# Kernel optimization log

Hardware: AMD Instinct MI355X
Metric: run time of the kernel (lower is better)

The kernel has to match this reference:

```python
import jax, jax.numpy as jnp
import numpy as np

ALPHA = 32.0 ** 2
MASK_VALUE = -jnp.finfo(jnp.float32).max


def rotate_half(t):
    d = t.shape[-1] // 2
    x1, x2 = t[..., :d], t[..., d:]
    return jnp.concatenate([-x2, x1], axis=-1)


def apply_rotary_pos_emb(freqs, t):
    # freqs: [n, rot_dim], t: [b, h, n, d]
    rot_dim = freqs.shape[-1]
    t_rot, t_pass = t[..., :rot_dim], t[..., rot_dim:]
    t_rot = t_rot * jnp.cos(freqs) + rotate_half(t_rot) * jnp.sin(freqs)
    return jnp.concatenate([t_rot, t_pass], axis=-1)


def stable_softmax(t, alpha=ALPHA):
    t = t / alpha
    t = t - jax.lax.stop_gradient(jnp.max(t, axis=-1, keepdims=True))
    return jax.nn.softmax(t * alpha, axis=-1)


def setup_inputs() -> dict:
    key = jax.random.key(0)
    ks = jax.random.split(key, 8)
    b, n, dim = 2, 2048, 1024
    h, dh = 16, 64
    inner = h * dh
    rot_dim = 32
    return {
        "x": jax.random.normal(ks[0], (b, n, dim), jnp.float32),
        "mask": jnp.ones((b, n), dtype=bool),
        "rotary_pos_emb": jax.random.normal(ks[1], (n, rot_dim), jnp.float32),
        "null_k": jax.random.normal(ks[2], (h, 1, dh), jnp.float32),
        "null_v": jax.random.normal(ks[3], (h, 1, dh), jnp.float32),
        "th_w": jax.random.normal(ks[4], (h, h), jnp.float32) * (1.0 / h),
        "w_q": jax.random.normal(ks[5], (dim, inner), jnp.float32) * (dim ** -0.5),
        "w_kv": jax.random.normal(ks[6], (dim, 2 * inner), jnp.float32) * (dim ** -0.5),
        "w_out": jax.random.normal(ks[7], (inner, dim), jnp.float32) * (inner ** -0.5),
        "b_out": jnp.zeros((dim,), jnp.float32),
    }


def reference(x, mask, rotary_pos_emb, null_k, null_v, th_w, w_q, w_kv, w_out, b_out):
    b, n, _ = x.shape
    h, _, dh = null_k.shape
    scale = dh ** -0.5

    q = x @ w_q                      # [b, n, h*dh]
    kv = x @ w_kv                    # [b, n, 2*h*dh]
    k, v = jnp.split(kv, 2, axis=-1)

    def to_heads(t):
        return t.reshape(b, n, h, dh).transpose(0, 2, 1, 3)  # [b, h, n, d]

    q, k, v = map(to_heads, (q, k, v))

    # rotary applied to q, k AND v (as in source)
    q = apply_rotary_pos_emb(rotary_pos_emb, q)
    k = apply_rotary_pos_emb(rotary_pos_emb, k)
    v = apply_rotary_pos_emb(rotary_pos_emb, v)

    # prepend learned null key/value token
    nk = jnp.broadcast_to(null_k[None], (b, h, 1, dh))
    nv = jnp.broadcast_to(null_v[None], (b, h, 1, dh))
    k = jnp.concatenate([nk, k], axis=2)  # [b, h, n+1, d]
    v = jnp.concatenate([nv, v], axis=2)

    q = q * scale
    sim = jnp.einsum('bhid,bhjd->bhij', q, k)  # [b, h, n, n+1]

    # key padding mask (null token always visible)
    key_mask = jnp.pad(mask, ((0, 0), (1, 0)), constant_values=True)
    sim = jnp.where(key_mask[:, None, None, :], sim, MASK_VALUE)

    # causal mask: padded col > row + (j - i)
    i, j = sim.shape[-2], sim.shape[-1]
    causal = jnp.arange(j)[None, :] > jnp.arange(i)[:, None] + (j - i)
    sim = jnp.where(causal, MASK_VALUE, sim)

    attn = stable_softmax(sim)
    # talking heads: 1x1 conv over head channel == head mixing matrix
    attn = jnp.einsum('gh,bhij->bgij', th_w, attn)

    out = jnp.einsum('bhij,bhjd->bhid', attn, v)
    out = out.transpose(0, 2, 1, 3).reshape(b, n, h * dh)
    return out @ w_out + b_out
```

## Files before the change

### kernel.cpp

```cpp
#include <hip/hip_runtime.h>
#include <hip/hip_bf16.h>
#include <cstdint>
#include <cstddef>

using bf16 = __hip_bfloat16;
typedef __attribute__((ext_vector_type(8))) short short8;
typedef __attribute__((ext_vector_type(4))) short short4v;
typedef __attribute__((ext_vector_type(4))) float f32x4;

constexpr int BB  = 2;
constexpr int SEQ = 2048;
constexpr int NH  = 16;
constexpr int HD  = 64;
constexpr int KPAD = 2112;
constexpr int DM  = 1024;

static __device__ __forceinline__ bf16 f2b(float v) { return __float2bfloat16(v); }
static __device__ __forceinline__ float b2f(bf16 v) { return __bfloat162float(v); }

static __device__ __forceinline__ void gload16(const bf16* g, bf16* l) {
  __builtin_amdgcn_global_load_lds(
      (const __attribute__((address_space(1))) void*)g,
      (__attribute__((address_space(3))) void*)l, 16, 0, 0);
}

__global__ __launch_bounds__(256) void cast_x_kernel(const float* __restrict__ src,
                                                     bf16* __restrict__ dst, int n4) {
  int idx = blockIdx.x * 256 + threadIdx.x;
  if (idx >= n4) return;
  float4 v = *(const float4*)(src + (size_t)idx * 4);
  bf16 o[4] = {f2b(v.x), f2b(v.y), f2b(v.z), f2b(v.w)};
  *(short4v*)(dst + (size_t)idx * 4) = *(short4v*)o;
}

__global__ __launch_bounds__(256) void zero_kernel(float* __restrict__ dst, int n4) {
  int idx = blockIdx.x * 256 + threadIdx.x;
  if (idx >= n4) return;
  float4 z; z.x = 0.f; z.y = 0.f; z.z = 0.f; z.w = 0.f;
  *(float4*)(dst + (size_t)idx * 4) = z;
}

__global__ __launch_bounds__(256) void cast_o_kernel(const float* __restrict__ src,
                                                     bf16* __restrict__ dst, int n4) {
  int idx = blockIdx.x * 256 + threadIdx.x;
  if (idx >= n4) return;
  float4 v = *(const float4*)(src + (size_t)idx * 4);
  bf16 o[4] = {f2b(v.x), f2b(v.y), f2b(v.z), f2b(v.w)};
  *(short4v*)(dst + (size_t)idx * 4) = *(short4v*)o;
}

__global__ __launch_bounds__(256) void transpose_cast_kernel(const float* __restrict__ src,
                                                             bf16* __restrict__ dst,
                                                             int colsN, int ldDst) {
  int n0 = blockIdx.x * 32, k0 = blockIdx.y * 32;
  __shared__ alignas(16) float t[32][33];
  int tid = threadIdx.x;
  {
    int r = tid >> 3, c4 = (tid & 7) * 4;
    float4 v = *(const float4*)(src + (size_t)(k0 + r) * colsN + n0 + c4);
    t[r][c4 + 0] = v.x; t[r][c4 + 1] = v.y; t[r][c4 + 2] = v.z; t[r][c4 + 3] = v.w;
  }
  __syncthreads();
  {
    int nl = tid >> 3, k4 = (tid & 7) * 4;
    bf16 o[4];
#pragma unroll
    for (int u = 0; u < 4; ++u) o[u] = f2b(t[k4 + u][nl]);
    *(short4v*)(dst + (size_t)(n0 + nl) * ldDst + k0 + k4) = *(short4v*)o;
  }
}

template <bool OUT_BF16, bool BIAS>
__global__ __launch_bounds__(256) void gemm_lds_kernel(
    const bf16* __restrict__ A, int lda,
    const bf16* __restrict__ BT, int ldb,
    void* __restrict__ Cv, int ldc,
    const float* __restrict__ bias, int K) {
  constexpr int BK = 32;
  const int tid = threadIdx.x, wave = tid >> 6, lane = tid & 63;
  const int lr = lane & 15, lq = lane >> 4;
  const int wm = wave >> 1, wn = wave & 1;
  const int m0 = blockIdx.y * 128, n0 = blockIdx.x * 128;
  const int srow = lane >> 2;
  const int scol = (lane & 3) * 8;

  __shared__ alignas(16) bf16 ash[128 * BK];
  __shared__ alignas(16) bf16 bsh[128 * BK];

  f32x4 acc[4][4];
#pragma unroll
  for (int i = 0; i < 4; ++i)
#pragma unroll
    for (int j = 0; j < 4; ++j)
#pragma unroll
      for (int r = 0; r < 4; ++r) acc[i][j][r] = 0.f;

  const int nk = K / BK;
  for (int kt = 0; kt < nk; ++kt) {
    const int k0 = kt * BK;
#pragma unroll
    for (int c = 0; c < 2; ++c) {
      const int rbase = wave * 32 + c * 16;
      gload16(A + (size_t)(m0 + rbase + srow) * lda + k0 + scol, ash + rbase * BK);
      gload16(BT + (size_t)(n0 + rbase + srow) * ldb + k0 + scol, bsh + rbase * BK);
    }
    __syncthreads();
    short8 af[4], bfv[4];
#pragma unroll
    for (int i = 0; i < 4; ++i)
      af[i] = *(const short8*)&ash[(wm * 64 + i * 16 + lr) * BK + lq * 8];
#pragma unroll
    for (int j = 0; j < 4; ++j)
      bfv[j] = *(const short8*)&bsh[(wn * 64 + j * 16 + lr) * BK + lq * 8];
#pragma unroll
    for (int i = 0; i < 4; ++i)
#pragma unroll
      for (int j = 0; j < 4; ++j)
        acc[i][j] = __builtin_amdgcn_mfma_f32_16x16x32_bf16(af[i], bfv[j], acc[i][j], 0, 0, 0);
    __syncthreads();
  }
#pragma unroll
  for (int i = 0; i < 4; ++i) {
    int row0 = m0 + wm * 64 + i * 16 + lq * 4;
#pragma unroll
    for (int j = 0; j < 4; ++j) {
      int col = n0 + wn * 64 + j * 16 + lr;
      float bv = BIAS ? bias[col] : 0.f;
#pragma unroll
      for (int r = 0; r < 4; ++r) {
        float v = acc[i][j][r] + bv;
        if (OUT_BF16) ((bf16*)Cv)[(size_t)(row0 + r) * ldc + col] = f2b(v);
        else          ((float*)Cv)[(size_t)(row0 + r) * ldc + col] = v;
      }
    }
  }
}

template <int BM, int BN, int BK, int WM, int WN, bool OUT_BF16, bool BIAS>
__global__ __launch_bounds__(WM * WN * 64) void gemm_bt_kernel(
    const bf16* __restrict__ A, int lda,
    const bf16* __restrict__ BT, int ldb,
    void* __restrict__ Cv, int ldc,
    const float* __restrict__ bias, int K) {
  constexpr int THREADS = WM * WN * 64;
  constexpr int FM = BM / (WM * 16), FN = BN / (WN * 16);
  const int tid = threadIdx.x;
  const int wave = tid >> 6, lane = tid & 63;
  const int lr = lane & 15, lq = lane >> 4;
  const int wm = wave / WN, wn = wave % WN;
  const int m0 = blockIdx.y * BM, n0 = blockIdx.x * BN;

  __shared__ alignas(16) bf16 ash[BM][BK + 8];
  __shared__ alignas(16) bf16 bsh[BN][BK + 8];

  f32x4 acc[FM][FN];
#pragma unroll
  for (int i = 0; i < FM; ++i)
#pragma unroll
    for (int j = 0; j < FN; ++j)
#pragma unroll
      for (int r = 0; r < 4; ++r) acc[i][j][r] = 0.f;

  const int nk = K / BK;
  for (int kt = 0; kt < nk; ++kt) {
    const int k0 = kt * BK;
#pragma unroll
    for (int c = 0; c < (BM * BK / 8) / THREADS; ++c) {
      int idx = tid + c * THREADS;
      int row = idx / (BK / 8), kc = (idx % (BK / 8)) * 8;
      *(short8*)&ash[row][kc] = *(const short8*)(A + (size_t)(m0 + row) * lda + k0 + kc);
    }
#pragma unroll
    for (int c = 0; c < (BN * BK / 8) / THREADS; ++c) {
      int idx = tid + c * THREADS;
      int row = idx / (BK / 8), kc = (idx % (BK / 8)) * 8;
      *(short8*)&bsh[row][kc] = *(const short8*)(BT + (size_t)(n0 + row) * ldb + k0 + kc);
    }
    __syncthreads();
    short8 af[FM], bfv[FN];
#pragma unroll
    for (int i = 0; i < FM; ++i)
      af[i] = *(const short8*)&ash[wm * FM * 16 + i * 16 + lr][lq * 8];
#pragma unroll
    for (int j = 0; j < FN; ++j)
      bfv[j] = *(const short8*)&bsh[wn * FN * 16 + j * 16 + lr][lq * 8];
#pragma unroll
    for (int i = 0; i < FM; ++i)
#pragma unroll
      for (int j = 0; j < FN; ++j)
        acc[i][j] = __builtin_amdgcn_mfma_f32_16x16x32_bf16(af[i], bfv[j], acc[i][j], 0, 0, 0);
    __syncthreads();
  }
#pragma unroll
  for (int i = 0; i < FM; ++i) {
    int row0 = m0 + wm * FM * 16 + i * 16 + lq * 4;
#pragma unroll
    for (int j = 0; j < FN; ++j) {
      int col = n0 + wn * FN * 16 + j * 16 + lr;
      float bv = BIAS ? bias[col] : 0.f;
#pragma unroll
      for (int r = 0; r < 4; ++r) {
        float v = acc[i][j][r] + bv;
        if (OUT_BF16) ((bf16*)Cv)[(size_t)(row0 + r) * ldc + col] = f2b(v);
        else          ((float*)Cv)[(size_t)(row0 + r) * ldc + col] = v;
      }
    }
  }
}

__global__ __launch_bounds__(256) void rope_build_kernel(
    const bf16* __restrict__ qkv, const float* __restrict__ rot,
    const float* __restrict__ nullk, const float* __restrict__ nullv,
    bf16* __restrict__ Q, bf16* __restrict__ Kt, bf16* __restrict__ Vt) {
  const int blk = blockIdx.x;
  const int ic = blk & 63;
  const int h = (blk >> 6) & 15;
  const int b = blk >> 10;
  const int i0 = ic * 32;
  const int tid = threadIdx.x;
  const int bh = b * NH + h;

  __shared__ alignas(16) bf16 sh[33][192];
  __shared__ alignas(16) float cs[33][32], sn[33][32];

  for (int c = 0; c < 4; ++c) {
    int idx = tid + c * 256;
    if (idx < 33 * 24) {
      int row = idx / 24, ch = idx % 24;
      int p = ch >> 3, cc = (ch & 7) * 8;
      int i = i0 - 1 + row;
      if (i >= 0)
        *(short8*)&sh[row][p * 64 + cc] =
            *(const short8*)(qkv + (size_t)(b * SEQ + i) * 3072 + p * 1024 + h * 64 + cc);
    }
  }
  for (int c = 0; c < 5; ++c) {
    int idx = tid + c * 256;
    if (idx < 33 * 32) {
      int row = idx >> 5, d = idx & 31;
      int i = i0 - 1 + row;
      if (i >= 0) {
        float f = rot[i * 32 + d];
        cs[row][d] = cosf(f);
        sn[row][d] = sinf(f);
      }
    }
  }
  __syncthreads();

  auto ropev = [&](int row, int off, int d) -> float {
    float v = b2f(sh[row][off + d]);
    if (d < 32) {
      float c = cs[row][d], s = sn[row][d];
      float v2 = b2f(sh[row][off + (d < 16 ? d + 16 : d - 16)]);
      return d < 16 ? v * c - v2 * s : v * c + v2 * s;
    }
    return v;
  };

  const int dA = tid & 63;
#pragma unroll
  for (int rep = 0; rep < 8; ++rep) {
    int il = rep * 4 + (tid >> 6);
    int row = il + 1;
    int i = i0 + il;
    float qv = ropev(row, 0, dA) * 0.125f;
    float kv = ropev(row, 64, dA);
    Q[((size_t)bh * SEQ + i) * HD + dA] = f2b(qv);
    Kt[((size_t)bh * KPAD + (i + 1)) * HD + dA] = f2b(kv);
  }
  {
    int d = tid >> 2;
    int g0 = (tid & 3) * 8;
    bf16 tmp[8];
#pragma unroll
    for (int u = 0; u < 8; ++u) {
      int j = i0 + g0 + u;
      if (j == 0) tmp[u] = f2b(nullv[h * 64 + d]);
      else        tmp[u] = f2b(ropev(j - i0, 128, d));
    }
    *(short8*)(Vt + ((size_t)bh * HD + d) * KPAD + i0 + g0) = *(short8*)tmp;
  }
  if (i0 == 0 && tid < 64)
    Kt[(size_t)bh * KPAD * HD + tid] = f2b(nullk[h * 64 + tid]);
  if (ic == 63 && tid < 64)
    Vt[((size_t)bh * HD + tid) * KPAD + 2048] = f2b(ropev(32, 128, tid));
}

__global__ __launch_bounds__(256) void denom_kernel(
    const bf16* __restrict__ Q, const bf16* __restrict__ Kt, float* __restrict__ Linv) {
  const int bh = blockIdx.x;
  const int i0 = blockIdx.y * 32;
  const int tid = threadIdx.x;
  const int wave = tid >> 6, lane = tid & 63;
  const int lr = lane & 15, lq = lane >> 4;
  const bf16* Qp = Q + (size_t)bh * SEQ * HD;
  const bf16* Kp = Kt + (size_t)bh * KPAD * HD;

  short8 af[2][2];
#pragma unroll
  for (int fi = 0; fi < 2; ++fi)
#pragma unroll
    for (int ks = 0; ks < 2; ++ks)
      af[fi][ks] = *(const short8*)(Qp + (size_t)(i0 + fi * 16 + lr) * HD + ks * 32 + lq * 8);

  const int tmax = (i0 + 32) >> 6;
  float lacc[2][4];
#pragma unroll
  for (int fi = 0; fi < 2; ++fi)
#pragma unroll
    for (int r = 0; r < 4; ++r) lacc[fi][r] = 0.f;

  for (int t = wave; t <= tmax; t += 4) {
    f32x4 s[2][4];
#pragma unroll
    for (int fi = 0; fi < 2; ++fi)
#pragma unroll
      for (int fj = 0; fj < 4; ++fj)
#pragma unroll
        for (int r = 0; r < 4; ++r) s[fi][fj][r] = 0.f;
#pragma unroll
    for (int fj = 0; fj < 4; ++fj) {
      const bf16* kp = Kp + (size_t)(t * 64 + fj * 16 + lr) * HD + lq * 8;
      short8 b0 = *(const short8*)kp;
      short8 b1 = *(const short8*)(kp + 32);
#pragma unroll
      for (int fi = 0; fi < 2; ++fi) {
        s[fi][fj] = __builtin_amdgcn_mfma_f32_16x16x32_bf16(af[fi][0], b0, s[fi][fj], 0, 0, 0);
        s[fi][fj] = __builtin_amdgcn_mfma_f32_16x16x32_bf16(af[fi][1], b1, s[fi][fj], 0, 0, 0);
      }
    }
#pragma unroll
    for (int fi = 0; fi < 2; ++fi)
#pragma unroll
      for (int fj = 0; fj < 4; ++fj)
#pragma unroll
        for (int r = 0; r < 4; ++r) {
          int i = i0 + fi * 16 + lq * 4 + r;
          int j = t * 64 + fj * 16 + lr;
          if (j <= i + 1) lacc[fi][r] += __expf(s[fi][fj][r]);
        }
  }
#pragma unroll
  for (int m = 1; m <= 8; m <<= 1)
#pragma unroll
    for (int fi = 0; fi < 2; ++fi)
#pragma unroll
      for (int r = 0; r < 4; ++r) lacc[fi][r] += __shfl_xor(lacc[fi][r], m, 64);

  __shared__ alignas(16) float lsh[4][32];
  if (lr == 0) {
#pragma unroll
    for (int fi = 0; fi < 2; ++fi)
#pragma unroll
      for (int r = 0; r < 4; ++r) lsh[wave][fi * 16 + lq * 4 + r] = lacc[fi][r];
  }
  __syncthreads();
  if (tid < 32)
    Linv[(size_t)bh * SEQ + i0 + tid] =
        1.f / (lsh[0][tid] + lsh[1][tid] + lsh[2][tid] + lsh[3][tid]);
}

__global__ __launch_bounds__(512) void fused2_kernel(
    const bf16* __restrict__ Q, const bf16* __restrict__ Kt, const bf16* __restrict__ Vt,
    const float* __restrict__ Linv, const float* __restrict__ thw,
    float* __restrict__ ohf) {
  const int pairIdx = blockIdx.x >> 3;
  const int b  = (blockIdx.x >> 2) & 1;
  const int jq = blockIdx.x & 3;
  const int tid = threadIdx.x;
  const int w = tid >> 6, lane = tid & 63;
  const int lr = lane & 15, lq = lane >> 4;

  __shared__ alignas(16) bf16 p_sh[1024 * 20];
  __shared__ alignas(16) bf16 p2[16 * 1024];

  short8 zero8;
#pragma unroll
  for (int e = 0; e < 8; ++e) zero8[e] = 0;
  f32x4 fzero;
#pragma unroll
  for (int r = 0; r < 4; ++r) fzero[r] = 0.f;

  short8 wfrag = zero8;
  if (lq < 2) {
    bf16 tmp[8];
#pragma unroll
    for (int e = 0; e < 8; ++e) tmp[e] = f2b(thw[lr * 16 + lq * 8 + e]);
    wfrag = *(short8*)tmp;
  }

#pragma unroll
  for (int sel = 0; sel < 2; ++sel) {
    const int ic = sel ? 127 - pairIdx : pairIdx;
    const int i0 = ic * 16;
    const int n = ((i0 + 16) >> 6) + 1;
    const int t0 = (n * jq) >> 2;
    const int t1 = (n * (jq + 1)) >> 2;

    short8 qf[2][2];
    float linv[2][4];
    const bf16* Vp[2];
    const bf16* Kp[2];
#pragma unroll
    for (int hh = 0; hh < 2; ++hh) {
      const int h = w + hh * 8;
      const int bh = b * NH + h;
      const bf16* Qp = Q + ((size_t)bh * SEQ + i0) * HD;
#pragma unroll
      for (int ks = 0; ks < 2; ++ks)
        qf[hh][ks] = *(const short8*)(Qp + (size_t)lr * HD + ks * 32 + lq * 8);
#pragma unroll
      for (int r = 0; r < 4; ++r)
        linv[hh][r] = Linv[(size_t)bh * SEQ + i0 + lq * 4 + r];
      Kp[hh] = Kt + (size_t)bh * KPAD * HD;
      Vp[hh] = Vt + (size_t)bh * HD * KPAD;
    }

    f32x4 oacc[2][4];
#pragma unroll
    for (int hh = 0; hh < 2; ++hh)
#pragma unroll
      for (int fn = 0; fn < 4; ++fn) oacc[hh][fn] = fzero;

    for (int t = t0; t < t1; ++t) {
#pragma unroll
      for (int hh = 0; hh < 2; ++hh) {
        const int h = w + hh * 8;
        f32x4 s[4];
#pragma unroll
        for (int fj = 0; fj < 4; ++fj) s[fj] = fzero;
#pragma unroll
        for (int fj = 0; fj < 4; ++fj) {
          const bf16* kp = Kp[hh] + (size_t)(t * 64 + fj * 16 + lr) * HD + lq * 8;
          short8 b0 = *(const short8*)kp;
          short8 b1 = *(const short8*)(kp + 32);
          s[fj] = __builtin_amdgcn_mfma_f32_16x16x32_bf16(qf[hh][0], b0, s[fj], 0, 0, 0);
          s[fj] = __builtin_amdgcn_mfma_f32_16x16x32_bf16(qf[hh][1], b1, s[fj], 0, 0, 0);
        }
#pragma unroll
        for (int fj = 0; fj < 4; ++fj)
#pragma unroll
          for (int r = 0; r < 4; ++r) {
            int il = lq * 4 + r;
            int jl = fj * 16 + lr;
            int i = i0 + il, j = t * 64 + jl;
            float p = (j <= i + 1) ? __expf(s[fj][r]) * linv[hh][r] : 0.f;
            p_sh[(il * 64 + jl) * 20 + h] = f2b(p);
          }
      }
      __syncthreads();
#pragma unroll
      for (int q = 0; q < 8; ++q) {
        const int c = (w * 8 + q) * 16 + lr;
        short8 bfrag = zero8;
        if (lq < 2) {
          short4v lo = *(const short4v*)&p_sh[c * 20 + lq * 8];
          short4v hi = *(const short4v*)&p_sh[c * 20 + lq * 8 + 4];
#pragma unroll
          for (int e = 0; e < 4; ++e) { bfrag[e] = lo[e]; bfrag[4 + e] = hi[e]; }
        }
        f32x4 d = __builtin_amdgcn_mfma_f32_16x16x32_bf16(wfrag, bfrag, fzero, 0, 0, 0);
        const int sc = c ^ (((c >> 6) & 7) << 3);
#pragma unroll
        for (int r = 0; r < 4; ++r)
          p2[(lq * 4 + r) * 1024 + sc] = f2b(d[r]);
      }
      __syncthreads();
#pragma unroll
      for (int hh = 0; hh < 2; ++hh) {
        const int h = w + hh * 8;
        short8 pa[2];
#pragma unroll
        for (int ks = 0; ks < 2; ++ks) {
          const int c = lr * 64 + ks * 32 + lq * 8;
          const int sc = c ^ (((c >> 6) & 7) << 3);
          pa[ks] = *(const short8*)&p2[h * 1024 + sc];
        }
#pragma unroll
        for (int fn = 0; fn < 4; ++fn) {
          const bf16* vp = Vp[hh] + (size_t)(fn * 16 + lr) * KPAD + t * 64 + lq * 8;
          short8 v0 = *(const short8*)vp;
          short8 v1 = *(const short8*)(vp + 32);
          oacc[hh][fn] = __builtin_amdgcn_mfma_f32_16x16x32_bf16(pa[0], v0, oacc[hh][fn], 0, 0, 0);
          oacc[hh][fn] = __builtin_amdgcn_mfma_f32_16x16x32_bf16(pa[1], v1, oacc[hh][fn], 0, 0, 0);
        }
      }
    }
#pragma unroll
    for (int hh = 0; hh < 2; ++hh) {
      const int h = w + hh * 8;
#pragma unroll
      for (int fn = 0; fn < 4; ++fn)
#pragma unroll
        for (int r = 0; r < 4; ++r)
          atomicAdd(ohf + (size_t)(b * SEQ + i0 + lq * 4 + r) * DM + h * 64 + fn * 16 + lr,
                    oacc[hh][fn][r]);
    }
    __syncthreads();
  }
}

extern "C" void kernel_launch(void* const* d_in, const int* in_sizes, int n_in,
                              void* d_out, int out_size, void* d_ws, size_t ws_size,
                              hipStream_t stream) {
  const float* x     = (const float*)d_in[0];
  const float* rot   = (const float*)d_in[2];
  const float* nullk = (const float*)d_in[3];
  const float* nullv = (const float*)d_in[4];
  const float* thw   = (const float*)d_in[5];
  const float* wq    = (const float*)d_in[6];
  const float* wkv   = (const float*)d_in[7];
  const float* wout  = (const float*)d_in[8];
  const float* bout  = (const float*)d_in[9];
  float* out = (float*)d_out;

  char* ws = (char*)d_ws;
  size_t off = 0;
  auto alloc = [&](size_t bytes) { char* p = ws + off; off += (bytes + 255) & ~(size_t)255; return p; };
  bf16* x_bf    = (bf16*)alloc((size_t)BB * SEQ * DM * 2);
  bf16* wqkv_t  = (bf16*)alloc((size_t)3072 * 1024 * 2);
  bf16* wout_t  = (bf16*)alloc((size_t)1024 * 1024 * 2);
  bf16* qkv_bf  = (bf16*)alloc((size_t)BB * SEQ * 3072 * 2);
  bf16* Qb      = (bf16*)alloc((size_t)BB * NH * SEQ * HD * 2);
  bf16* Kt      = (bf16*)alloc((size_t)BB * NH * KPAD * HD * 2);
  bf16* Vt      = (bf16*)alloc((size_t)BB * NH * HD * KPAD * 2);
  float* Linv   = (float*)alloc((size_t)BB * NH * SEQ * 4);
  bf16* oh      = (bf16*)alloc((size_t)BB * SEQ * DM * 2);
  (void)ws_size;
  float* ohf = (float*)qkv_bf;

  cast_x_kernel<<<(BB * SEQ * DM / 4 + 255) / 256, 256, 0, stream>>>(x, x_bf, BB * SEQ * DM / 4);
  transpose_cast_kernel<<<dim3(1024 / 32, 1024 / 32), 256, 0, stream>>>(wq, wqkv_t, 1024, 1024);
  transpose_cast_kernel<<<dim3(2048 / 32, 1024 / 32), 256, 0, stream>>>(wkv, wqkv_t + (size_t)1024 * 1024, 2048, 1024);
  transpose_cast_kernel<<<dim3(1024 / 32, 1024 / 32), 256, 0, stream>>>(wout, wout_t, 1024, 1024);

  gemm_lds_kernel<true, false>
      <<<dim3(3072 / 128, 4096 / 128), 256, 0, stream>>>(
          x_bf, 1024, wqkv_t, 1024, qkv_bf, 3072, nullptr, 1024);

  rope_build_kernel<<<BB * NH * (SEQ / 32), 256, 0, stream>>>(qkv_bf, rot, nullk, nullv, Qb, Kt, Vt);

  zero_kernel<<<(BB * SEQ * DM / 4 + 255) / 256, 256, 0, stream>>>(ohf, BB * SEQ * DM / 4);

  denom_kernel<<<dim3(BB * NH, SEQ / 32), 256, 0, stream>>>(Qb, Kt, Linv);

  fused2_kernel<<<512, 512, 0, stream>>>(Qb, Kt, Vt, Linv, thw, ohf);

  cast_o_kernel<<<(BB * SEQ * DM / 4 + 255) / 256, 256, 0, stream>>>(ohf, oh, BB * SEQ * DM / 4);

  gemm_bt_kernel<128, 128, 32, 2, 2, false, true>
      <<<dim3(1024 / 128, 4096 / 128), 256, 0, stream>>>(
          oh, 1024, wout_t, 1024, out, 1024, bout, 1024);
}
```

Measured before the change: 422.2 us.

## Materialize head-mixed probabilities to workspace and run separate PV GEMM

```diff
diff --git a/kernel.cpp b/kernel.cpp
--- a/kernel.cpp
+++ b/kernel.cpp
@@ -136,78 +136,6 @@
   }
 }
 
-template <int BM, int BN, int BK, int WM, int WN, bool OUT_BF16, bool BIAS>
-__global__ __launch_bounds__(WM * WN * 64) void gemm_bt_kernel(
-    const bf16* __restrict__ A, int lda,
-    const bf16* __restrict__ BT, int ldb,
-    void* __restrict__ Cv, int ldc,
-    const float* __restrict__ bias, int K) {
-  constexpr int THREADS = WM * WN * 64;
-  constexpr int FM = BM / (WM * 16), FN = BN / (WN * 16);
-  const int tid = threadIdx.x;
-  const int wave = tid >> 6, lane = tid & 63;
-  const int lr = lane & 15, lq = lane >> 4;
-  const int wm = wave / WN, wn = wave % WN;
-  const int m0 = blockIdx.y * BM, n0 = blockIdx.x * BN;
-
-  __shared__ alignas(16) bf16 ash[BM][BK + 8];
-  __shared__ alignas(16) bf16 bsh[BN][BK + 8];
-
-  f32x4 acc[FM][FN];
-#pragma unroll
-  for (int i = 0; i < FM; ++i)
-#pragma unroll
-    for (int j = 0; j < FN; ++j)
-#pragma unroll
-      for (int r = 0; r < 4; ++r) acc[i][j][r] = 0.f;
-
-  const int nk = K / BK;
-  for (int kt = 0; kt < nk; ++kt) {
-    const int k0 = kt * BK;
-#pragma unroll
-    for (int c = 0; c < (BM * BK / 8) / THREADS; ++c) {
-      int idx = tid + c * THREADS;
-      int row = idx / (BK / 8), kc = (idx % (BK / 8)) * 8;
-      *(short8*)&ash[row][kc] = *(const short8*)(A + (size_t)(m0 + row) * lda + k0 + kc);
-    }
-#pragma unroll
-    for (int c = 0; c < (BN * BK / 8) / THREADS; ++c) {
-      int idx = tid + c * THREADS;
-      int row = idx / (BK / 8), kc = (idx % (BK / 8)) * 8;
-      *(short8*)&bsh[row][kc] = *(const short8*)(BT + (size_t)(n0 + row) * ldb + k0 + kc);
-    }
-    __syncthreads();
-    short8 af[FM], bfv[FN];
-#pragma unroll
-    for (int i = 0; i < FM; ++i)
-      af[i] = *(const short8*)&ash[wm * FM * 16 + i * 16 + lr][lq * 8];
-#pragma unroll
-    for (int j = 0; j < FN; ++j)
-      bfv[j] = *(const short8*)&bsh[wn * FN * 16 + j * 16 + lr][lq * 8];
-#pragma unroll
-    for (int i = 0; i < FM; ++i)
-#pragma unroll
-      for (int j = 0; j < FN; ++j)
-        acc[i][j] = __builtin_amdgcn_mfma_f32_16x16x32_bf16(af[i], bfv[j], acc[i][j], 0, 0, 0);
-    __syncthreads();
-  }
-#pragma unroll
-  for (int i = 0; i < FM; ++i) {
-    int row0 = m0 + wm * FM * 16 + i * 16 + lq * 4;
-#pragma unroll
-    for (int j = 0; j < FN; ++j) {
-      int col = n0 + wn * FN * 16 + j * 16 + lr;
-      float bv = BIAS ? bias[col] : 0.f;
-#pragma unroll
-      for (int r = 0; r < 4; ++r) {
-        float v = acc[i][j][r] + bv;
-        if (OUT_BF16) ((bf16*)Cv)[(size_t)(row0 + r) * ldc + col] = f2b(v);
-        else          ((float*)Cv)[(size_t)(row0 + r) * ldc + col] = v;
-      }
-    }
-  }
-}
-
 __global__ __launch_bounds__(256) void rope_build_kernel(
     const bf16* __restrict__ qkv, const float* __restrict__ rot,
     const float* __restrict__ nullk, const float* __restrict__ nullv,
@@ -361,19 +289,165 @@
         1.f / (lsh[0][tid] + lsh[1][tid] + lsh[2][tid] + lsh[3][tid]);
 }
 
+__global__ __launch_bounds__(256) void pmix_kernel(
+    const bf16* __restrict__ Q, const bf16* __restrict__ Kt,
+    const float* __restrict__ Linv, const float* __restrict__ thw,
+    bf16* __restrict__ Pm) {
+  const int t = blockIdx.x;
+  const int ic = blockIdx.y;
+  const int i0 = ic * 32;
+  const int tid = threadIdx.x, wave = tid >> 6, lane = tid & 63;
+  const int lr = lane & 15, lq = lane >> 4;
+  const int tmax = (i0 + 32) >> 6;
+
+  short8 zero8;
+#pragma unroll
+  for (int e = 0; e < 8; ++e) zero8[e] = 0;
+
+  if (t > tmax) {
+    if (t > (ic >> 1) + 1) return;
+#pragma unroll
+    for (int k = 0; k < 16; ++k) {
+      int idx = tid + k * 256;
+      int g = idx >> 8, rest = idx & 255;
+      int il = rest >> 3, jc = (rest & 7) * 8;
+      *(short8*)(Pm + ((size_t)g * SEQ + i0 + il) * KPAD + t * 64 + jc) = zero8;
+    }
+    return;
+  }
+
+  __shared__ alignas(16) bf16 p_sh[2048][16];
+
+  f32x4 fzero;
+#pragma unroll
+  for (int r = 0; r < 4; ++r) fzero[r] = 0.f;
+
+  short8 wfrag = zero8;
+  if (lq < 2) {
+    bf16 tmp[8];
+#pragma unroll
+    for (int e = 0; e < 8; ++e) tmp[e] = f2b(thw[lr * 16 + lq * 8 + e]);
+    wfrag = *(short8*)tmp;
+  }
+
+#pragma unroll
+  for (int hh = 0; hh < 4; ++hh) {
+    const int h = wave * 4 + hh;
+    const bf16* Qp = Q + ((size_t)h * SEQ + i0) * HD;
+    const bf16* Kp = Kt + ((size_t)h * KPAD + t * 64) * HD;
+    short8 qf[2][2];
+#pragma unroll
+    for (int fi = 0; fi < 2; ++fi)
+#pragma unroll
+      for (int ks = 0; ks < 2; ++ks)
+        qf[fi][ks] = *(const short8*)(Qp + (size_t)(fi * 16 + lr) * HD + ks * 32 + lq * 8);
+    float linv[2][4];
+#pragma unroll
+    for (int fi = 0; fi < 2; ++fi)
+#pragma unroll
+      for (int r = 0; r < 4; ++r)
+        linv[fi][r] = Linv[(size_t)h * SEQ + i0 + fi * 16 + lq * 4 + r];
+
+    f32x4 s[2][4];
+#pragma unroll
+    for (int fi = 0; fi < 2; ++fi)
+#pragma unroll
+      for (int fj = 0; fj < 4; ++fj) s[fi][fj] = fzero;
+#pragma unroll
+    for (int fj = 0; fj < 4; ++fj) {
+      const bf16* kp = Kp + (size_t)(fj * 16 + lr) * HD + lq * 8;
+      short8 b0 = *(const short8*)kp;
+      short8 b1 = *(const short8*)(kp + 32);
+#pragma unroll
+      for (int fi = 0; fi < 2; ++fi) {
+        s[fi][fj] = __builtin_amdgcn_mfma_f32_16x16x32_bf16(qf[fi][0], b0, s[fi][fj], 0, 0, 0);
+        s[fi][fj] = __builtin_amdgcn_mfma_f32_16x16x32_bf16(qf[fi][1], b1, s[fi][fj], 0, 0, 0);
+      }
+    }
+#pragma unroll
+    for (int fi = 0; fi < 2; ++fi)
+#pragma unroll
+      for (int fj = 0; fj < 4; ++fj)
+#pragma unroll
+        for (int r = 0; r < 4; ++r) {
+          int il = fi * 16 + lq * 4 + r;
+          int jl = fj * 16 + lr;
+          int i = i0 + il, j = t * 64 + jl;
+          float p = (j <= i + 1) ? __expf(s[fi][fj][r]) * linv[fi][r] : 0.f;
+          p_sh[il * 64 + jl][h] = f2b(p);
+        }
+  }
+  __syncthreads();
+
+#pragma unroll
+  for (int q = 0; q < 32; ++q) {
+    const int c = (wave * 32 + q) * 16 + lr;
+    short8 bfrag = zero8;
+    if (lq < 2) bfrag = *(const short8*)&p_sh[c][lq * 8];
+    f32x4 d = __builtin_amdgcn_mfma_f32_16x16x32_bf16(wfrag, bfrag, fzero, 0, 0, 0);
+    const int il = c >> 6, jl = c & 63;
+#pragma unroll
+    for (int r = 0; r < 4; ++r) {
+      const int g = lq * 4 + r;
+      Pm[((size_t)g * SEQ + i0 + il) * KPAD + t * 64 + jl] = f2b(d[r]);
+    }
+  }
+}
+
+__global__ __launch_bounds__(256) void pv64_kernel(
+    const bf16* __restrict__ Pm, const bf16* __restrict__ Vt, bf16* __restrict__ oh) {
+  const int g = blockIdx.x;
+  const int m0 = blockIdx.y * 64;
+  const int tid = threadIdx.x, w = tid >> 6, lane = tid & 63;
+  const int lr = lane & 15, lq = lane >> 4;
+  const bf16* A  = Pm + (size_t)g * SEQ * KPAD;
+  const bf16* BT = Vt + (size_t)g * HD * KPAD;
+
+  __shared__ alignas(16) bf16 ash[64][40];
+  __shared__ alignas(16) bf16 bsh[64][40];
+
+  f32x4 acc[4];
+#pragma unroll
+  for (int j = 0; j < 4; ++j)
+#pragma unroll
+    for (int r = 0; r < 4; ++r) acc[j][r] = 0.f;
+
+  const int nk = m0 / 32 + 3;
+  for (int kt = 0; kt < nk; ++kt) {
+    const int k0 = kt * 32;
+    *(short8*)&ash[tid >> 2][(tid & 3) * 8] =
+        *(const short8*)(A + (size_t)(m0 + (tid >> 2)) * KPAD + k0 + (tid & 3) * 8);
+    *(short8*)&bsh[tid >> 2][(tid & 3) * 8] =
+        *(const short8*)(BT + (size_t)(tid >> 2) * KPAD + k0 + (tid & 3) * 8);
+    __syncthreads();
+    short8 af = *(const short8*)&ash[w * 16 + lr][lq * 8];
+#pragma unroll
+    for (int j = 0; j < 4; ++j) {
+      short8 bfv = *(const short8*)&bsh[j * 16 + lr][lq * 8];
+      acc[j] = __builtin_amdgcn_mfma_f32_16x16x32_bf16(af, bfv, acc[j], 0, 0, 0);
+    }
+    __syncthreads();
+  }
+#pragma unroll
+  for (int j = 0; j < 4; ++j)
+#pragma unroll
+    for (int r = 0; r < 4; ++r)
+      oh[(size_t)(m0 + w * 16 + lq * 4 + r) * DM + g * 64 + j * 16 + lr] = f2b(acc[j][r]);
+}
+
 __global__ __launch_bounds__(512) void fused2_kernel(
     const bf16* __restrict__ Q, const bf16* __restrict__ Kt, const bf16* __restrict__ Vt,
     const float* __restrict__ Linv, const float* __restrict__ thw,
     float* __restrict__ ohf) {
-  const int pairIdx = blockIdx.x >> 3;
-  const int b  = (blockIdx.x >> 2) & 1;
-  const int jq = blockIdx.x & 3;
+  const int pairIdx = blockIdx.x >> 2;
+  const int b  = (blockIdx.x >> 1) & 1;
+  const int jh = blockIdx.x & 1;
   const int tid = threadIdx.x;
   const int w = tid >> 6, lane = tid & 63;
   const int lr = lane & 15, lq = lane >> 4;
 
-  __shared__ alignas(16) bf16 p_sh[1024 * 20];
-  __shared__ alignas(16) bf16 p2[16 * 1024];
+  __shared__ alignas(16) bf16 p_sh[1024 * 24];
+  __shared__ alignas(16) bf16 p2[16 * 1032];
 
   short8 zero8;
 #pragma unroll
@@ -395,8 +469,9 @@
     const int ic = sel ? 127 - pairIdx : pairIdx;
     const int i0 = ic * 16;
     const int n = ((i0 + 16) >> 6) + 1;
-    const int t0 = (n * jq) >> 2;
-    const int t1 = (n * (jq + 1)) >> 2;
+    const int half = (n + 1) >> 1;
+    const int t0 = jh ? half : 0;
+    const int t1 = jh ? n : half;
 
     short8 qf[2][2];
     float linv[2][4];
@@ -446,7 +521,7 @@
             int jl = fj * 16 + lr;
             int i = i0 + il, j = t * 64 + jl;
             float p = (j <= i + 1) ? __expf(s[fj][r]) * linv[hh][r] : 0.f;
-            p_sh[(il * 64 + jl) * 20 + h] = f2b(p);
+            p_sh[(il * 64 + jl) * 24 + h] = f2b(p);
           }
       }
       __syncthreads();
@@ -454,17 +529,12 @@
       for (int q = 0; q < 8; ++q) {
         const int c = (w * 8 + q) * 16 + lr;
         short8 bfrag = zero8;
-        if (lq < 2) {
-          short4v lo = *(const short4v*)&p_sh[c * 20 + lq * 8];
-          short4v hi = *(const short4v*)&p_sh[c * 20 + lq * 8 + 4];
-#pragma unroll
-          for (int e = 0; e < 4; ++e) { bfrag[e] = lo[e]; bfrag[4 + e] = hi[e]; }
-        }
+        if (lq < 2) bfrag = *(const short8*)&p_sh[c * 24 + lq * 8];
         f32x4 d = __builtin_amdgcn_mfma_f32_16x16x32_bf16(wfrag, bfrag, fzero, 0, 0, 0);
         const int sc = c ^ (((c >> 6) & 7) << 3);
 #pragma unroll
         for (int r = 0; r < 4; ++r)
-          p2[(lq * 4 + r) * 1024 + sc] = f2b(d[r]);
+          p2[(lq * 4 + r) * 1032 + sc] = f2b(d[r]);
       }
       __syncthreads();
 #pragma unroll
@@ -475,7 +545,7 @@
         for (int ks = 0; ks < 2; ++ks) {
           const int c = lr * 64 + ks * 32 + lq * 8;
           const int sc = c ^ (((c >> 6) & 7) << 3);
-          pa[ks] = *(const short8*)&p2[h * 1024 + sc];
+          pa[ks] = *(const short8*)&p2[h * 1032 + sc];
         }
 #pragma unroll
         for (int fn = 0; fn < 4; ++fn) {
@@ -521,13 +591,16 @@
   bf16* x_bf    = (bf16*)alloc((size_t)BB * SEQ * DM * 2);
   bf16* wqkv_t  = (bf16*)alloc((size_t)3072 * 1024 * 2);
   bf16* wout_t  = (bf16*)alloc((size_t)1024 * 1024 * 2);
-  bf16* qkv_bf  = (bf16*)alloc((size_t)BB * SEQ * 3072 * 2);
   bf16* Qb      = (bf16*)alloc((size_t)BB * NH * SEQ * HD * 2);
   bf16* Kt      = (bf16*)alloc((size_t)BB * NH * KPAD * HD * 2);
   bf16* Vt      = (bf16*)alloc((size_t)BB * NH * HD * KPAD * 2);
   float* Linv   = (float*)alloc((size_t)BB * NH * SEQ * 4);
   bf16* oh      = (bf16*)alloc((size_t)BB * SEQ * DM * 2);
-  (void)ws_size;
+  const size_t shared_off = off;
+  bf16* qkv_bf = (bf16*)(ws + shared_off);
+  bf16* Pm     = (bf16*)(ws + shared_off);
+  const size_t PM_BYTES = (size_t)NH * SEQ * KPAD * 2;
+  const bool pathA = (shared_off + PM_BYTES) <= ws_size;
   float* ohf = (float*)qkv_bf;
 
   cast_x_kernel<<<(BB * SEQ * DM / 4 + 255) / 256, 256, 0, stream>>>(x, x_bf, BB * SEQ * DM / 4);
@@ -541,15 +614,24 @@
 
   rope_build_kernel<<<BB * NH * (SEQ / 32), 256, 0, stream>>>(qkv_bf, rot, nullk, nullv, Qb, Kt, Vt);
 
-  zero_kernel<<<(BB * SEQ * DM / 4 + 255) / 256, 256, 0, stream>>>(ohf, BB * SEQ * DM / 4);
-
   denom_kernel<<<dim3(BB * NH, SEQ / 32), 256, 0, stream>>>(Qb, Kt, Linv);
 
-  fused2_kernel<<<512, 512, 0, stream>>>(Qb, Kt, Vt, Linv, thw, ohf);
-
-  cast_o_kernel<<<(BB * SEQ * DM / 4 + 255) / 256, 256, 0, stream>>>(ohf, oh, BB * SEQ * DM / 4);
-
-  gemm_bt_kernel<128, 128, 32, 2, 2, false, true>
+  if (pathA) {
+    for (int b = 0; b < BB; ++b) {
+      pmix_kernel<<<dim3(33, 64), 256, 0, stream>>>(
+          Qb + (size_t)b * NH * SEQ * HD,
+          Kt + (size_t)b * NH * KPAD * HD,
+          Linv + (size_t)b * NH * SEQ, thw, Pm);
+      pv64_kernel<<<dim3(16, 32), 256, 0, stream>>>(
+          Pm, Vt + (size_t)b * NH * HD * KPAD, oh + (size_t)b * SEQ * DM);
+    }
+  } else {
+    zero_kernel<<<(BB * SEQ * DM / 4 + 255) / 256, 256, 0, stream>>>(ohf, BB * SEQ * DM / 4);
+    fused2_kernel<<<256, 512, 0, stream>>>(Qb, Kt, Vt, Linv, thw, ohf);
+    cast_o_kernel<<<(BB * SEQ * DM / 4 + 255) / 256, 256, 0, stream>>>(ohf, oh, BB * SEQ * DM / 4);
+  }
+
+  gemm_lds_kernel<false, true>
       <<<dim3(1024 / 128, 4096 / 128), 256, 0, stream>>>(
           oh, 1024, wout_t, 1024, out, 1024, bout, 1024);
 }
```

After: 399.2 us. 1.06x faster.
